# Kernel optimization log

Hardware: AMD Instinct MI355X
Metric: run time of the kernel (lower is better)

The kernel has to match this reference:

```python
import jax, jax.numpy as jnp
import numpy as np
from jax import lax

WINDOW_SIZE = 11
SIGMA = 1.5
DATA_RANGE = 2.0


def _gauss_1d(size, sigma):
    coords = np.arange(size, dtype=np.float32) - size // 2
    g = np.exp(-coords ** 2 / (2.0 * sigma ** 2))
    return jnp.asarray(g / g.sum())


def _gaussian_filter(x, win):
    C = x.shape[1]
    K = win.shape[0]
    pad = K // 2
    dn = ('NCHW', 'OIHW', 'NCHW')
    kh = jnp.tile(win.reshape(1, 1, 1, K), (C, 1, 1, 1)).astype(x.dtype)
    kv = jnp.tile(win.reshape(1, 1, K, 1), (C, 1, 1, 1)).astype(x.dtype)
    out = lax.conv_general_dilated(x, kh, window_strides=(1, 1),
                                   padding=[(0, 0), (pad, pad)],
                                   dimension_numbers=dn, feature_group_count=C)
    out = lax.conv_general_dilated(out, kv, window_strides=(1, 1),
                                   padding=[(pad, pad), (0, 0)],
                                   dimension_numbers=dn, feature_group_count=C)
    return out


def setup_inputs() -> dict:
    key = jax.random.key(0)
    k1, k2 = jax.random.split(key)
    pred = jax.random.normal(k1, (32, 3, 512, 512), dtype=jnp.float32)
    target = jax.random.normal(k2, (32, 3, 512, 512), dtype=jnp.float32)
    return {"pred": pred, "target": target}


def reference(pred, target):
    C1 = (0.01 * DATA_RANGE) ** 2
    C2 = (0.03 * DATA_RANGE) ** 2
    win = _gauss_1d(WINDOW_SIZE, SIGMA)
    mu_x = _gaussian_filter(pred, win)
    mu_y = _gaussian_filter(target, win)
    mu_x_sq = mu_x * mu_x
    mu_y_sq = mu_y * mu_y
    mu_xy = mu_x * mu_y
    sigma_x_sq = jnp.maximum(_gaussian_filter(pred * pred, win) - mu_x_sq, 0.0)
    sigma_y_sq = jnp.maximum(_gaussian_filter(target * target, win) - mu_y_sq, 0.0)
    sigma_xy = _gaussian_filter(pred * target, win) - mu_xy
    ssim_map = ((2.0 * mu_xy + C1) * (2.0 * sigma_xy + C2)) / (
        (mu_x_sq + mu_y_sq + C1) * (sigma_x_sq + sigma_y_sq + C2))
    return 1.0 - jnp.mean(ssim_map)
```

## Files before the change

### kernel.cpp

```cpp
#include <hip/hip_runtime.h>
#include <math.h>

#define IMG_H 512
#define IMG_W 512
#define NIMG 96
#define BH 64
#define NBANDS 8
#define ROWS_IN (BH + 10)
#define NCHUNK 7
#define SSTR 528
#define HOFF 6

__global__ __launch_bounds__(256, 2)
void ssim_main(const float* __restrict__ Pg, const float* __restrict__ Tg,
               float* __restrict__ acc) {
    __shared__ float sP[2 * SSTR];
    __shared__ float sT[2 * SSTR];
    __shared__ float wavesum[4];

    const int t = threadIdx.x;
    const int R0 = blockIdx.x * BH;
    const size_t plane = (size_t)blockIdx.y * (IMG_H * IMG_W);
    const float* P = Pg + plane;
    const float* T = Tg + plane;

    float w[11];
    {
        float s = 0.f;
#pragma unroll
        for (int k = 0; k < 11; ++k) {
            const float d = (float)(k - 5);
            w[k] = expf(-d * d / 4.5f);
            s += w[k];
        }
        const float inv = 1.0f / s;
#pragma unroll
        for (int k = 0; k < 11; ++k) w[k] *= inv;
    }

    if (t < 6) {
#pragma unroll
        for (int b = 0; b < 2; ++b) {
            sP[b * SSTR + t] = 0.f;
            sT[b * SSTR + t] = 0.f;
            sP[b * SSTR + 518 + t] = 0.f;
            sT[b * SSTR + 518 + t] = 0.f;
        }
    }

    float2 pv = {0.f, 0.f}, tv = {0.f, 0.f};
    {
        const int gr0 = R0 - 5;
        if (gr0 >= 0) {
            pv = *(const float2*)(P + (size_t)gr0 * IMG_W + 2 * t);
            tv = *(const float2*)(T + (size_t)gr0 * IMG_W + 2 * t);
        }
    }

    float bP[2][11], bT[2][11], bPP[2][11], bTT[2][11], bPT[2][11];
    float ssum = 0.f;

    for (int j = 0; j < NCHUNK; ++j) {
#pragma unroll
        for (int s = 0; s < 11; ++s) {
            const int li = 11 * j + s;
            if (li < ROWS_IN) {
                float* SPb = sP + (li & 1) * SSTR;
                float* STb = sT + (li & 1) * SSTR;
                *(float2*)(SPb + HOFF + 2 * t) = pv;
                *(float2*)(STb + HOFF + 2 * t) = tv;

                {
                    const int grn = R0 - 5 + li + 1;
                    float2 np = {0.f, 0.f}, nt = {0.f, 0.f};
                    if (li + 1 < ROWS_IN && grn >= 0 && grn < IMG_H) {
                        np = *(const float2*)(P + (size_t)grn * IMG_W + 2 * t);
                        nt = *(const float2*)(T + (size_t)grn * IMG_W + 2 * t);
                    }
                    pv = np; tv = nt;
                }

                __syncthreads();

                float p[14], q[14];
#pragma unroll
                for (int k = 0; k < 7; ++k) {
                    const float2 a = *(const float2*)(SPb + 2 * t + 2 * k);
                    const float2 b = *(const float2*)(STb + 2 * t + 2 * k);
                    p[2 * k] = a.x; p[2 * k + 1] = a.y;
                    q[2 * k] = b.x; q[2 * k + 1] = b.y;
                }

                float h00 = 0, h01 = 0, h02 = 0, h03 = 0, h04 = 0;
                float h10 = 0, h11 = 0, h12 = 0, h13 = 0, h14 = 0;
#pragma unroll
                for (int i = 1; i <= 12; ++i) {
                    const float ppv = p[i] * p[i];
                    const float ttv = q[i] * q[i];
                    const float ptv = p[i] * q[i];
                    if (i <= 11) {
                        const float wk = w[i - 1];
                        h00 = fmaf(wk, p[i], h00);
                        h01 = fmaf(wk, q[i], h01);
                        h02 = fmaf(wk, ppv, h02);
                        h03 = fmaf(wk, ttv, h03);
                        h04 = fmaf(wk, ptv, h04);
                    }
                    if (i >= 2) {
                        const float wk = w[i - 2];
                        h10 = fmaf(wk, p[i], h10);
                        h11 = fmaf(wk, q[i], h11);
                        h12 = fmaf(wk, ppv, h12);
                        h13 = fmaf(wk, ttv, h13);
                        h14 = fmaf(wk, ptv, h14);
                    }
                }
                bP[0][s] = h00; bT[0][s] = h01; bPP[0][s] = h02; bTT[0][s] = h03; bPT[0][s] = h04;
                bP[1][s] = h10; bT[1][s] = h11; bPP[1][s] = h12; bTT[1][s] = h13; bPT[1][s] = h14;

                if (li >= 10) {
#pragma unroll
                    for (int c = 0; c < 2; ++c) {
                        float mx = 0, my = 0, vxx = 0, vyy = 0, vxy = 0;
#pragma unroll
                        for (int k = 0; k < 11; ++k) {
                            const int sl = (s + 1 + k) % 11;
                            const float wk = w[k];
                            mx  = fmaf(wk, bP[c][sl],  mx);
                            my  = fmaf(wk, bT[c][sl],  my);
                            vxx = fmaf(wk, bPP[c][sl], vxx);
                            vyy = fmaf(wk, bTT[c][sl], vyy);
                            vxy = fmaf(wk, bPT[c][sl], vxy);
                        }
                        const float C1 = 4.0e-4f;
                        const float C2 = 3.6e-3f;
                        const float mxx = mx * mx, myy = my * my, mxy = mx * my;
                        const float sx = fmaxf(vxx - mxx, 0.f);
                        const float sy = fmaxf(vyy - myy, 0.f);
                        const float sxy = vxy - mxy;
                        const float num = fmaf(2.f, mxy, C1) * fmaf(2.f, sxy, C2);
                        const float den = (mxx + myy + C1) * (sx + sy + C2);
                        float r = __builtin_amdgcn_rcpf(den);
                        r = r * fmaf(-den, r, 2.0f);
                        ssum += num * r;
                    }
                }
            }
        }
    }

#pragma unroll
    for (int off = 32; off > 0; off >>= 1) ssum += __shfl_down(ssum, off);
    if ((t & 63) == 0) wavesum[t >> 6] = ssum;
    __syncthreads();
    if (t == 0) {
        atomicAdd(acc, wavesum[0] + wavesum[1] + wavesum[2] + wavesum[3]);
    }
}

__global__ void ssim_final(const float* __restrict__ acc, float* __restrict__ out) {
    out[0] = 1.0f - acc[0] / 25165824.0f;
}

extern "C" void kernel_launch(void* const* d_in, const int* in_sizes, int n_in,
                              void* d_out, int out_size, void* d_ws, size_t ws_size,
                              hipStream_t stream) {
    const float* pred = (const float*)d_in[0];
    const float* targ = (const float*)d_in[1];
    float* acc = (float*)d_ws;

    hipMemsetAsync(d_ws, 0, sizeof(float), stream);
    dim3 grid(NBANDS, NIMG);
    ssim_main<<<grid, 256, 0, stream>>>(pred, targ, acc);
    ssim_final<<<1, 1, 0, stream>>>(acc, (float*)d_out);
}
```

Baseline: 267.6 us.

## Read rows directly from global memory, drop LDS staging and halve band height

Replaces the double-buffered shared-memory row staging and per-row __syncthreads with direct global float2 loads of each thread's 14-column halo window, relying on L1/L2 to absorb the overlapping reads. Band height goes from 64 to 32 rows, doubling the grid, and launch bounds rise to 4 blocks per SM to improve occupancy. This removes barrier stalls and LDS traffic. In exchange it issues 7x more global load instructions per row, loses the one-row prefetch, and raises vertical halo overhead from 10/64 to 10/32 rows.

```diff
diff --git a/kernel.cpp b/kernel.cpp
--- a/kernel.cpp
+++ b/kernel.cpp
@@ -4,18 +4,14 @@
 #define IMG_H 512
 #define IMG_W 512
 #define NIMG 96
-#define BH 64
-#define NBANDS 8
+#define BH 32
+#define NBANDS 16
 #define ROWS_IN (BH + 10)
-#define NCHUNK 7
-#define SSTR 528
-#define HOFF 6
+#define NCHUNK 4
 
-__global__ __launch_bounds__(256, 2)
+__global__ __launch_bounds__(256, 4)
 void ssim_main(const float* __restrict__ Pg, const float* __restrict__ Tg,
                float* __restrict__ acc) {
-    __shared__ float sP[2 * SSTR];
-    __shared__ float sT[2 * SSTR];
     __shared__ float wavesum[4];
 
     const int t = threadIdx.x;
@@ -38,57 +34,36 @@
         for (int k = 0; k < 11; ++k) w[k] *= inv;
     }
 
-    if (t < 6) {
-#pragma unroll
-        for (int b = 0; b < 2; ++b) {
-            sP[b * SSTR + t] = 0.f;
-            sT[b * SSTR + t] = 0.f;
-            sP[b * SSTR + 518 + t] = 0.f;
-            sT[b * SSTR + 518 + t] = 0.f;
-        }
-    }
-
-    float2 pv = {0.f, 0.f}, tv = {0.f, 0.f};
-    {
-        const int gr0 = R0 - 5;
-        if (gr0 >= 0) {
-            pv = *(const float2*)(P + (size_t)gr0 * IMG_W + 2 * t);
-            tv = *(const float2*)(T + (size_t)gr0 * IMG_W + 2 * t);
-        }
-    }
-
     float bP[2][11], bT[2][11], bPP[2][11], bTT[2][11], bPT[2][11];
     float ssum = 0.f;
+
+    const int cbase = 2 * t - 6;
 
     for (int j = 0; j < NCHUNK; ++j) {
 #pragma unroll
         for (int s = 0; s < 11; ++s) {
             const int li = 11 * j + s;
             if (li < ROWS_IN) {
-                float* SPb = sP + (li & 1) * SSTR;
-                float* STb = sT + (li & 1) * SSTR;
-                *(float2*)(SPb + HOFF + 2 * t) = pv;
-                *(float2*)(STb + HOFF + 2 * t) = tv;
-
-                {
-                    const int grn = R0 - 5 + li + 1;
-                    float2 np = {0.f, 0.f}, nt = {0.f, 0.f};
-                    if (li + 1 < ROWS_IN && grn >= 0 && grn < IMG_H) {
-                        np = *(const float2*)(P + (size_t)grn * IMG_W + 2 * t);
-                        nt = *(const float2*)(T + (size_t)grn * IMG_W + 2 * t);
-                    }
-                    pv = np; tv = nt;
-                }
-
-                __syncthreads();
+                const int gr = R0 - 5 + li;
 
                 float p[14], q[14];
+                if (gr >= 0 && gr < IMG_H) {
+                    const float* Pr = P + (size_t)gr * IMG_W;
+                    const float* Tr = T + (size_t)gr * IMG_W;
 #pragma unroll
-                for (int k = 0; k < 7; ++k) {
-                    const float2 a = *(const float2*)(SPb + 2 * t + 2 * k);
-                    const float2 b = *(const float2*)(STb + 2 * t + 2 * k);
-                    p[2 * k] = a.x; p[2 * k + 1] = a.y;
-                    q[2 * k] = b.x; q[2 * k + 1] = b.y;
+                    for (int k = 0; k < 7; ++k) {
+                        const int c = cbase + 2 * k;
+                        float2 a = {0.f, 0.f}, b = {0.f, 0.f};
+                        if (c >= 0 && c < IMG_W) {
+                            a = *(const float2*)(Pr + c);
+                            b = *(const float2*)(Tr + c);
+                        }
+                        p[2 * k] = a.x; p[2 * k + 1] = a.y;
+                        q[2 * k] = b.x; q[2 * k + 1] = b.y;
+                    }
+                } else {
+#pragma unroll
+                    for (int k = 0; k < 14; ++k) { p[k] = 0.f; q[k] = 0.f; }
                 }
 
                 float h00 = 0, h01 = 0, h02 = 0, h03 = 0, h04 = 0;
```

Measured after the change: 754.3 us. 182% more time.
